# Kernel tuning notes

Measured on AMD Instinct MI355X. Metric: run time of the kernel, lower is better.

Reference implementation:

```python
import jax, jax.numpy as jnp
import numpy as np

BN_EPS = 1e-5
B, CIN, COUT, H, W, K, NSR = 16, 512, 512, 64, 64, 32, 6
M = NSR * K  # 192 codebook centers


def _l2norm(a, axis):
    return a / (1e-6 + jnp.linalg.norm(a, axis=axis, keepdims=True))


def _batchnorm(x, gamma, beta):
    # training-style BN over (batch, H, W), matching SynchronizedBatchNorm2d batch stats
    mean = x.mean(axis=(0, 2, 3), keepdims=True)
    var = x.var(axis=(0, 2, 3), keepdims=True)
    return gamma[None, :, None, None] * (x - mean) * jax.lax.rsqrt(var + BN_EPS) + beta[None, :, None, None]


def setup_inputs() -> dict:
    key = jax.random.key(0)
    ks = jax.random.split(key, 6)
    x = jax.random.normal(ks[0], (B, CIN, H, W), dtype=jnp.float32)
    centers = jax.random.normal(ks[1], (COUT, M), dtype=jnp.float32) * np.sqrt(2.0 / M)
    centers = _l2norm(centers, axis=0)
    # kaiming fan_out init for 1x1 convs
    conv1_w = jax.random.normal(ks[2], (COUT, CIN), dtype=jnp.float32) * np.sqrt(2.0 / COUT)
    conv1_b = jnp.zeros((COUT,), jnp.float32)
    conv2_w = jax.random.normal(ks[3], (CIN, COUT), dtype=jnp.float32) * np.sqrt(2.0 / CIN)
    bn2_g = jnp.ones((CIN,), jnp.float32)
    bn2_b = jnp.zeros((CIN,), jnp.float32)
    conv3_w = jax.random.normal(ks[4], (CIN, CIN), dtype=jnp.float32) * np.sqrt(2.0 / CIN)
    conv3_b = jnp.zeros((CIN,), jnp.float32)
    bn3_g = jnp.ones((CIN,), jnp.float32)
    bn3_b = jnp.zeros((CIN,), jnp.float32)
    return {"x": x, "centers": centers, "conv1_w": conv1_w, "conv1_b": conv1_b,
            "conv2_w": conv2_w, "bn2_g": bn2_g, "bn2_b": bn2_b,
            "conv3_w": conv3_w, "conv3_b": conv3_b, "bn3_g": bn3_g, "bn3_b": bn3_b}


def reference(x, centers, conv1_w, conv1_b, conv2_w, bn2_g, bn2_b, conv3_w, conv3_b, bn3_g, bn3_b):
    b, cin, h, w = x.shape
    # conv1: 1x1 projection in_channels -> out_channels
    x1 = jnp.einsum('oc,bchw->bohw', conv1_w, x) + conv1_b[None, :, None, None]
    x1f = x1.reshape(b, -1, h * w)  # [b, cout, n]
    # attention vs codebook (bases = centers, inference path period=None)
    att = jnp.einsum('bcn,ck->bnk', x1f, centers)  # [b, n, m]
    att = jax.nn.softmax(att, axis=2)
    # double normalization over spatial positions
    att = att / (1e-6 + att.sum(axis=1, keepdims=True))
    # reconstruction from codebook
    x_re = jnp.einsum('bnk,ck->bcn', att, centers).reshape(b, -1, h, w)  # [b, cout, h, w]
    # conv2: 1x1 (no bias) + BN + ReLU, out_channels -> in_channels
    x_re = jax.nn.relu(_batchnorm(jnp.einsum('oc,bchw->bohw', conv2_w, x_re), bn2_g, bn2_b))
    out = x_re + x  # residual
    # conv_bn_dropout: 1x1 conv + BN + ReLU (Dropout2d is identity at eval)
    out = jnp.einsum('oc,bchw->bohw', conv3_w, out) + conv3_b[None, :, None, None]
    out = jax.nn.relu(_batchnorm(out, bn3_g, bn3_b))
    return out
```

## Files before the change

kernel.cpp:

```cpp
#include <hip/hip_runtime.h>
#include <math.h>


#define B_    16
#define C_    512
#define N_    4096
#define M_    192
#define EPS_BN 1e-5f
#define CNT_  ((float)(B_ * N_))

typedef unsigned int   u32;
typedef unsigned short u16;
typedef short bf16x8 __attribute__((ext_vector_type(8)));
typedef float f32x4  __attribute__((ext_vector_type(4)));

__device__ __forceinline__ u16 bf16_rne(float f) {
  u32 u = __float_as_uint(f);
  u += 0x7FFFu + ((u >> 16) & 1u);
  return (u16)(u >> 16);
}
__device__ __forceinline__ float bf16_tof(u16 h) {
  return __uint_as_float(((u32)h) << 16);
}
__device__ __forceinline__ u32 split_pack(float v) {
  u16 h = bf16_rne(v);
  u16 l = bf16_rne(v - bf16_tof(h));
  return (u32)h | ((u32)l << 16);
}
__device__ __forceinline__ void split2(float a, float b, u32& h, u32& l) {
  u16 ha = bf16_rne(a), hb = bf16_rne(b);
  u16 la = bf16_rne(a - bf16_tof(ha)), lb = bf16_rne(b - bf16_tof(hb));
  h = (u32)ha | ((u32)hb << 16);
  l = (u32)la | ((u32)lb << 16);
}

__global__ __launch_bounds__(256) void convert_ew(
    const float* __restrict__ s, u16* __restrict__ hi, u16* __restrict__ lo) {
  const int i = (blockIdx.x * 256 + threadIdx.x) * 4;
  float4 v = *(const float4*)(s + i);
  u32 ph0, pl0, ph1, pl1;
  split2(v.x, v.y, ph0, pl0);
  split2(v.z, v.w, ph1, pl1);
  uint2 H; H.x = ph0; H.y = ph1;
  uint2 L; L.x = pl0; L.y = pl1;
  *(uint2*)(hi + i) = H;
  *(uint2*)(lo + i) = L;
}

__global__ __launch_bounds__(256) void convert_x_T(
    const float* __restrict__ X, u16* __restrict__ Thi, u16* __restrict__ Tlo) {
  __shared__ u32 T[64][65];
  const int tid = threadIdx.x;
  const int n0 = blockIdx.x * 64, c0 = blockIdx.y * 64, b = blockIdx.z;
  const int cg = (tid & 15) * 4;
#pragma unroll
  for (int p = 0; p < 4; ++p) {
    const int r = p * 16 + (tid >> 4);
    float4 v = *(const float4*)(X + ((size_t)b * C_ + c0 + r) * N_ + n0 + cg);
    T[r][cg + 0] = split_pack(v.x);
    T[r][cg + 1] = split_pack(v.y);
    T[r][cg + 2] = split_pack(v.z);
    T[r][cg + 3] = split_pack(v.w);
  }
  __syncthreads();
#pragma unroll
  for (int it = 0; it < 2; ++it) {
    const int s = it * 256 + tid;
    const int nl = s >> 3, cb = s & 7;
    u32 u[8];
#pragma unroll
    for (int j = 0; j < 8; ++j) u[j] = T[cb * 8 + j][nl];
    uint4 H, L;
    H.x = (u[0] & 0xFFFFu) | (u[1] << 16);
    H.y = (u[2] & 0xFFFFu) | (u[3] << 16);
    H.z = (u[4] & 0xFFFFu) | (u[5] << 16);
    H.w = (u[6] & 0xFFFFu) | (u[7] << 16);
    L.x = (u[0] >> 16) | (u[1] & 0xFFFF0000u);
    L.y = (u[2] >> 16) | (u[3] & 0xFFFF0000u);
    L.z = (u[4] >> 16) | (u[5] & 0xFFFF0000u);
    L.w = (u[6] >> 16) | (u[7] & 0xFFFF0000u);
    const size_t o = ((size_t)b * N_ + n0 + nl) * C_ + c0 + cb * 8;
    *(uint4*)(Thi + o) = H;
    *(uint4*)(Tlo + o) = L;
  }
}

__global__ __launch_bounds__(256) void conv_mfma(
    const u16* __restrict__ Whi, const u16* __restrict__ Wlo,
    const u16* __restrict__ Xhi, const u16* __restrict__ Xlo,
    float* __restrict__ Y, const float* __restrict__ bias) {
  __shared__ char sm[32768];
  const int tid = threadIdx.x, wid = tid >> 6, lane = tid & 63;
  const int bn = blockIdx.x * 128, bm = blockIdx.y * 128;
  const size_t boffX = (size_t)blockIdx.z * N_ * C_;
  const size_t boffY = (size_t)blockIdx.z * C_ * N_;

  const u16* srcp[8];
  u32 ldsw[8];
#pragma unroll
  for (int it = 0; it < 8; ++it) {
    const int lin = it * 4 + wid, region = lin >> 3, sub = lin & 7;
    const u16* base = region == 0 ? Whi : region == 1 ? Wlo
                    : region == 2 ? (Xhi + boffX) : (Xlo + boffX);
    const int rowb = (region < 2 ? bm : bn) + sub * 16 + (lane & 15);
    srcp[it] = base + (size_t)rowb * C_ + (lane >> 4) * 8;
    ldsw[it] = (u32)(lin * 1024 + lane * 16);
  }

  f32x4 acc[4][4];
  const f32x4 zero = {0.f, 0.f, 0.f, 0.f};
#pragma unroll
  for (int i = 0; i < 4; ++i)
#pragma unroll
    for (int j = 0; j < 4; ++j) acc[i][j] = zero;

  const int arow = (wid >> 1) * 4, bcol = (wid & 1) * 4;
  const char* smL = sm + lane * 16;

  for (int k0 = 0; k0 < C_; k0 += 32) {
    float4 stg[8];
#pragma unroll
    for (int it = 0; it < 8; ++it) stg[it] = *(const float4*)(srcp[it] + k0);
#pragma unroll
    for (int it = 0; it < 8; ++it) *(float4*)(sm + ldsw[it]) = stg[it];
    __syncthreads();

    bf16x8 ah[4], al[4], bh[4], bl[4];
#pragma unroll
    for (int i = 0; i < 4; ++i) {
      ah[i] = *(const bf16x8*)(smL + (arow + i) * 1024);
      al[i] = *(const bf16x8*)(smL + 8192 + (arow + i) * 1024);
      bh[i] = *(const bf16x8*)(smL + 16384 + (bcol + i) * 1024);
      bl[i] = *(const bf16x8*)(smL + 24576 + (bcol + i) * 1024);
    }
#pragma unroll
    for (int i = 0; i < 4; ++i)
#pragma unroll
      for (int j = 0; j < 4; ++j) {
        acc[i][j] = __builtin_amdgcn_mfma_f32_16x16x32_bf16(ah[i], bh[j], acc[i][j], 0, 0, 0);
        acc[i][j] = __builtin_amdgcn_mfma_f32_16x16x32_bf16(ah[i], bl[j], acc[i][j], 0, 0, 0);
        acc[i][j] = __builtin_amdgcn_mfma_f32_16x16x32_bf16(al[i], bh[j], acc[i][j], 0, 0, 0);
      }
    __syncthreads();
  }

  const int ro = (lane >> 4) * 4, co = lane & 15;
#pragma unroll
  for (int i = 0; i < 4; ++i) {
#pragma unroll
    for (int r = 0; r < 4; ++r) {
      const int o = bm + (wid >> 1) * 64 + i * 16 + ro + r;
      const float bv = bias ? bias[o] : 0.0f;
#pragma unroll
      for (int j = 0; j < 4; ++j) {
        const int n = bn + (wid & 1) * 64 + j * 16 + co;
        Y[boffY + (size_t)o * N_ + n] = acc[i][j][r] + bv;
      }
    }
  }
}

__global__ __launch_bounds__(256) void gemm_att(
    const float* __restrict__ X1, const float* __restrict__ Cent,
    float* __restrict__ Att) {
  const int tid = threadIdx.x;
  const int bn = blockIdx.x * 128;
  const int bk = blockIdx.y * 64;
  const float* Xb = X1 + (size_t)blockIdx.z * C_ * N_;

  __shared__ float As[8][128];
  __shared__ float Bs[8][64];

  float acc[8][4];
#pragma unroll
  for (int i = 0; i < 8; ++i)
#pragma unroll
    for (int j = 0; j < 4; ++j) acc[i][j] = 0.0f;

  const int tm = (tid >> 4) << 3;
  const int tn = (tid & 15) << 2;
  const int a_kc = tid >> 5;
  const int a_m4 = (tid & 31) << 2;
  const int b_kc = tid >> 5;
  const int b_c2 = (tid & 31) << 1;

  for (int k0 = 0; k0 < C_; k0 += 8) {
    *(float4*)&As[a_kc][a_m4] =
        *(const float4*)(Xb + (size_t)(k0 + a_kc) * N_ + bn + a_m4);
    *(float2*)&Bs[b_kc][b_c2] =
        *(const float2*)(Cent + (size_t)(k0 + b_kc) * M_ + bk + b_c2);
    __syncthreads();
#pragma unroll
    for (int kk = 0; kk < 8; ++kk) {
      float ar[8], br[4];
#pragma unroll
      for (int i = 0; i < 8; ++i) ar[i] = As[kk][tm + i];
#pragma unroll
      for (int j = 0; j < 4; ++j) br[j] = Bs[kk][tn + j];
#pragma unroll
      for (int i = 0; i < 8; ++i)
#pragma unroll
        for (int j = 0; j < 4; ++j) acc[i][j] = fmaf(ar[i], br[j], acc[i][j]);
    }
    __syncthreads();
  }

#pragma unroll
  for (int i = 0; i < 8; ++i) {
    float4 o = make_float4(acc[i][0], acc[i][1], acc[i][2], acc[i][3]);
    *(float4*)(Att + ((size_t)blockIdx.z * N_ + bn + tm + i) * M_ + bk + tn) = o;
  }
}

__global__ __launch_bounds__(256) void softmax_rows(float* __restrict__ Att) {
  const int wid  = threadIdx.x >> 6;
  const int lane = threadIdx.x & 63;
  const size_t row = (size_t)blockIdx.x * 4 + wid;
  float* p = Att + row * M_;
  float v0 = p[lane], v1 = p[lane + 64], v2 = p[lane + 128];
  float m = fmaxf(v0, fmaxf(v1, v2));
#pragma unroll
  for (int off = 32; off; off >>= 1) m = fmaxf(m, __shfl_xor(m, off));
  v0 = __expf(v0 - m);
  v1 = __expf(v1 - m);
  v2 = __expf(v2 - m);
  float s = v0 + v1 + v2;
#pragma unroll
  for (int off = 32; off; off >>= 1) s += __shfl_xor(s, off);
  const float r = 1.0f / s;
  p[lane]       = v0 * r;
  p[lane + 64]  = v1 * r;
  p[lane + 128] = v2 * r;
}

__global__ __launch_bounds__(256) void colsum_kernel(
    const float* __restrict__ Att, float* __restrict__ Cs) {
  const int b  = blockIdx.y;
  const int n0 = blockIdx.x * 256;
  const int k  = threadIdx.x;
  if (k < M_) {
    float s = 0.0f;
    const float* p = Att + ((size_t)b * N_ + n0) * M_ + k;
    for (int n = 0; n < 256; ++n) s += p[(size_t)n * M_];
    atomicAdd(&Cs[b * M_ + k], s);
  }
}

__global__ __launch_bounds__(256) void gemm_xre(
    const float* __restrict__ Cent, const float* __restrict__ Att,
    const float* __restrict__ Cs, u16* __restrict__ XThi, u16* __restrict__ XTlo) {
  const int tid = threadIdx.x;
  const int bn = blockIdx.x * 128;
  const int bm = blockIdx.y * 128;
  const int b  = blockIdx.z;

  __shared__ float As[8][128];
  __shared__ float Bs[8][128];
  __shared__ float inv[M_];

  if (tid < M_) inv[tid] = 1.0f / (1e-6f + Cs[b * M_ + tid]);
  __syncthreads();

  float acc[8][8];
#pragma unroll
  for (int i = 0; i < 8; ++i)
#pragma unroll
    for (int j = 0; j < 8; ++j) acc[i][j] = 0.0f;

  const int tm = (tid >> 4) << 3;
  const int tn = (tid & 15) << 3;
  const int a_row = tid >> 1;
  const int a_col = (tid & 1) << 2;
  const int b_row = tid >> 1;
  const int b_col = (tid & 1) << 2;

  for (int k0 = 0; k0 < M_; k0 += 8) {
    float4 av = *(const float4*)(Cent + (size_t)(bm + a_row) * M_ + k0 + a_col);
    As[a_col + 0][a_row] = av.x;
    As[a_col + 1][a_row] = av.y;
    As[a_col + 2][a_row] = av.z;
    As[a_col + 3][a_row] = av.w;
    float4 bv = *(const float4*)(Att + ((size_t)b * N_ + bn + b_row) * M_ + k0 + b_col);
    Bs[b_col + 0][b_row] = bv.x * inv[k0 + b_col + 0];
    Bs[b_col + 1][b_row] = bv.y * inv[k0 + b_col + 1];
    Bs[b_col + 2][b_row] = bv.z * inv[k0 + b_col + 2];
    Bs[b_col + 3][b_row] = bv.w * inv[k0 + b_col + 3];
    __syncthreads();
#pragma unroll
    for (int kk = 0; kk < 8; ++kk) {
      float ar[8], br[8];
#pragma unroll
      for (int i = 0; i < 8; ++i) ar[i] = As[kk][tm + i];
#pragma unroll
      for (int j = 0; j < 8; ++j) br[j] = Bs[kk][tn + j];
#pragma unroll
      for (int i = 0; i < 8; ++i)
#pragma unroll
        for (int j = 0; j < 8; ++j) acc[i][j] = fmaf(ar[i], br[j], acc[i][j]);
    }
    __syncthreads();
  }

#pragma unroll
  for (int jj = 0; jj < 8; ++jj) {
    uint4 H, L;
    split2(acc[0][jj], acc[1][jj], H.x, L.x);
    split2(acc[2][jj], acc[3][jj], H.y, L.y);
    split2(acc[4][jj], acc[5][jj], H.z, L.z);
    split2(acc[6][jj], acc[7][jj], H.w, L.w);
    const size_t o = ((size_t)b * N_ + bn + tn + jj) * C_ + bm + tm;
    *(uint4*)(XThi + o) = H;
    *(uint4*)(XTlo + o) = L;
  }
}

__global__ __launch_bounds__(256) void bnstats(
    const float* __restrict__ Y, float* __restrict__ stats) {
  const int c = blockIdx.x, b = blockIdx.y;
  const float4* p = (const float4*)(Y + ((size_t)b * C_ + c) * N_);
  float s = 0.0f, s2 = 0.0f;
  for (int i = threadIdx.x; i < N_ / 4; i += 256) {
    float4 v = p[i];
    s  += v.x + v.y + v.z + v.w;
    s2 += v.x * v.x + v.y * v.y + v.z * v.z + v.w * v.w;
  }
#pragma unroll
  for (int off = 32; off; off >>= 1) {
    s  += __shfl_xor(s, off);
    s2 += __shfl_xor(s2, off);
  }
  __shared__ float ws[2][4];
  const int lane = threadIdx.x & 63, wid = threadIdx.x >> 6;
  if (lane == 0) { ws[0][wid] = s; ws[1][wid] = s2; }
  __syncthreads();
  if (threadIdx.x == 0) {
    float ts = ws[0][0] + ws[0][1] + ws[0][2] + ws[0][3];
    float t2 = ws[1][0] + ws[1][1] + ws[1][2] + ws[1][3];
    atomicAdd(&stats[c], ts);
    atomicAdd(&stats[C_ + c], t2);
  }
}

__global__ __launch_bounds__(256) void bn_res_T(
    const float* __restrict__ Y, const float* __restrict__ X,
    const float* __restrict__ stats, const float* __restrict__ g,
    const float* __restrict__ bta,
    u16* __restrict__ Thi, u16* __restrict__ Tlo) {
  __shared__ u32 T[64][65];
  const int tid = threadIdx.x;
  const int n0 = blockIdx.x * 64, c0 = blockIdx.y * 64, b = blockIdx.z;
  const int cg = (tid & 15) * 4;
#pragma unroll
  for (int p = 0; p < 4; ++p) {
    const int r = p * 16 + (tid >> 4);
    const int c = c0 + r;
    const float mu  = stats[c] * (1.0f / CNT_);
    const float var = stats[C_ + c] * (1.0f / CNT_) - mu * mu;
    const float rs  = rsqrtf(var + EPS_BN);
    const float ga = g[c], be = bta[c];
    const size_t idx = ((size_t)b * C_ + c) * N_ + n0 + cg;
    float4 v  = *(const float4*)(Y + idx);
    float4 xv = *(const float4*)(X + idx);
    float4 t;
    t.x = fmaxf(ga * (v.x - mu) * rs + be, 0.0f) + xv.x;
    t.y = fmaxf(ga * (v.y - mu) * rs + be, 0.0f) + xv.y;
    t.z = fmaxf(ga * (v.z - mu) * rs + be, 0.0f) + xv.z;
    t.w = fmaxf(ga * (v.w - mu) * rs + be, 0.0f) + xv.w;
    T[r][cg + 0] = split_pack(t.x);
    T[r][cg + 1] = split_pack(t.y);
    T[r][cg + 2] = split_pack(t.z);
    T[r][cg + 3] = split_pack(t.w);
  }
  __syncthreads();
#pragma unroll
  for (int it = 0; it < 2; ++it) {
    const int s = it * 256 + tid;
    const int nl = s >> 3, cb = s & 7;
    u32 u[8];
#pragma unroll
    for (int j = 0; j < 8; ++j) u[j] = T[cb * 8 + j][nl];
    uint4 H, L;
    H.x = (u[0] & 0xFFFFu) | (u[1] << 16);
    H.y = (u[2] & 0xFFFFu) | (u[3] << 16);
    H.z = (u[4] & 0xFFFFu) | (u[5] << 16);
    H.w = (u[6] & 0xFFFFu) | (u[7] << 16);
    L.x = (u[0] >> 16) | (u[1] & 0xFFFF0000u);
    L.y = (u[2] >> 16) | (u[3] & 0xFFFF0000u);
    L.z = (u[4] >> 16) | (u[5] & 0xFFFF0000u);
    L.w = (u[6] >> 16) | (u[7] & 0xFFFF0000u);
    const size_t o = ((size_t)b * N_ + n0 + nl) * C_ + c0 + cb * 8;
    *(uint4*)(Thi + o) = H;
    *(uint4*)(Tlo + o) = L;
  }
}

__global__ __launch_bounds__(256) void bn_apply(
    const float* __restrict__ Y, const float* __restrict__ stats,
    const float* __restrict__ g, const float* __restrict__ bta,
    float* __restrict__ Out) {
  const size_t i = ((size_t)blockIdx.x * 256 + threadIdx.x) * 4;
  const int c = (int)((i >> 12) & (C_ - 1));
  const float mu  = stats[c] * (1.0f / CNT_);
  const float var = stats[C_ + c] * (1.0f / CNT_) - mu * mu;
  const float rs  = rsqrtf(var + EPS_BN);
  const float ga = g[c], be = bta[c];
  float4 y = *(const float4*)(Y + i);
  float4 o;
  o.x = fmaxf(ga * (y.x - mu) * rs + be, 0.0f);
  o.y = fmaxf(ga * (y.y - mu) * rs + be, 0.0f);
  o.z = fmaxf(ga * (y.z - mu) * rs + be, 0.0f);
  o.w = fmaxf(ga * (y.w - mu) * rs + be, 0.0f);
  *(float4*)(Out + i) = o;
}

__global__ __launch_bounds__(256) void zero_small(float* __restrict__ p) {
  p[blockIdx.x * 256 + threadIdx.x] = 0.0f;
}

extern "C" void kernel_launch(void* const* d_in, const int* in_sizes, int n_in,
                              void* d_out, int out_size, void* d_ws, size_t ws_size,
                              hipStream_t stream) {
  const float* x        = (const float*)d_in[0];
  const float* centers  = (const float*)d_in[1];
  const float* conv1_w  = (const float*)d_in[2];
  const float* conv1_b  = (const float*)d_in[3];
  const float* conv2_w  = (const float*)d_in[4];
  const float* bn2_g    = (const float*)d_in[5];
  const float* bn2_b    = (const float*)d_in[6];
  const float* conv3_w  = (const float*)d_in[7];
  const float* conv3_b  = (const float*)d_in[8];
  const float* bn3_g    = (const float*)d_in[9];
  const float* bn3_b    = (const float*)d_in[10];
  float* out = (float*)d_out;

  const size_t TENS = (size_t)B_ * C_ * N_;
  char* w = (char*)d_ws;
  u16* xThi = (u16*)w;
  u16* xTlo = xThi + TENS;
  float* x1 = (float*)(w + 134217728);
  float* att = (float*)(w + 268435456);
  float* colsum = (float*)(w + 268435456 + 50331648);
  float* stats2 = colsum + B_ * M_;
  float* stats3 = stats2 + 2 * C_;
  u16* w1hi = (u16*)(stats3 + 2 * C_);
  u16* w1lo = w1hi + 262144;
  u16* w2hi = w1lo + 262144;
  u16* w2lo = w2hi + 262144;
  u16* w3hi = w2lo + 262144;
  u16* w3lo = w3hi + 262144;
  u16* xreThi = xThi;  u16* xreTlo = xTlo;
  u16* tThi   = xThi;  u16* tTlo   = xTlo;
  float* y2 = x1;

  zero_small<<<20, 256, 0, stream>>>(colsum);
  convert_ew<<<256, 256, 0, stream>>>(conv1_w, w1hi, w1lo);
  convert_ew<<<256, 256, 0, stream>>>(conv2_w, w2hi, w2lo);
  convert_ew<<<256, 256, 0, stream>>>(conv3_w, w3hi, w3lo);
  convert_x_T<<<dim3(N_ / 64, C_ / 64, B_), 256, 0, stream>>>(x, xThi, xTlo);
  conv_mfma<<<dim3(N_ / 128, C_ / 128, B_), 256, 0, stream>>>(
      w1hi, w1lo, xThi, xTlo, x1, conv1_b);
  gemm_att<<<dim3(N_ / 128, M_ / 64, B_), 256, 0, stream>>>(x1, centers, att);
  softmax_rows<<<(B_ * N_) / 4, 256, 0, stream>>>(att);
  colsum_kernel<<<dim3(16, B_), 256, 0, stream>>>(att, colsum);
  gemm_xre<<<dim3(N_ / 128, C_ / 128, B_), 256, 0, stream>>>(
      centers, att, colsum, xreThi, xreTlo);
  conv_mfma<<<dim3(N_ / 128, C_ / 128, B_), 256, 0, stream>>>(
      w2hi, w2lo, xreThi, xreTlo, y2, nullptr);
  bnstats<<<dim3(C_, B_), 256, 0, stream>>>(y2, stats2);
  bn_res_T<<<dim3(N_ / 64, C_ / 64, B_), 256, 0, stream>>>(
      y2, x, stats2, bn2_g, bn2_b, tThi, tTlo);
  conv_mfma<<<dim3(N_ / 128, C_ / 128, B_), 256, 0, stream>>>(
      w3hi, w3lo, tThi, tTlo, out, conv3_b);
  bnstats<<<dim3(C_, B_), 256, 0, stream>>>(out, stats3);
  bn_apply<<<(B_ * C_ * N_) / (4 * 256), 256, 0, stream>>>(
      out, stats3, bn3_g, bn3_b, out);
}
```

Baseline: 1.186 ms.

## Move attention and reconstruction GEMMs to split-bf16 MFMA with fused softmax and colsum

Replaces the fp32 FMA attention GEMM, the separate softmax and colsum kernels, and the fp32 reconstruction GEMM with MFMA kernels using hi/lo bf16 splitting. The conv1 output is now written transposed as split bf16, so the attention kernel computes all 192 logits per position and applies softmax and column-sum atomics in registers. The reconstruction step folds the column normalization into a per-batch scaled copy of the centers and runs through a templated MFMA GEMM. This removes several full passes over the attention tensor and moves slow scalar GEMMs onto matrix cores. The trade-offs are extra atomics, higher register pressure in the attention kernel, and small rounding differences from the 3-term bf16 split.

Measured after the change: 1.120 ms. -5.6%, faster.

```diff
diff --git a/kernel.cpp b/kernel.cpp
--- a/kernel.cpp
+++ b/kernel.cpp
@@ -45,6 +45,32 @@
   uint2 L; L.x = pl0; L.y = pl1;
   *(uint2*)(hi + i) = H;
   *(uint2*)(lo + i) = L;
+}
+
+__global__ __launch_bounds__(256) void centT_conv(
+    const float* __restrict__ cent, u16* __restrict__ hi, u16* __restrict__ lo) {
+  const int idx = blockIdx.x * 256 + threadIdx.x;
+  const int k = idx >> 9, c = idx & 511;
+  const float v = cent[c * M_ + k];
+  u16 h = bf16_rne(v);
+  u16 l = bf16_rne(v - bf16_tof(h));
+  hi[idx] = h;
+  lo[idx] = l;
+}
+
+__global__ __launch_bounds__(256) void cent_scale(
+    const float* __restrict__ cent, const float* __restrict__ colsum,
+    u16* __restrict__ hi, u16* __restrict__ lo) {
+  const int idx = blockIdx.x * 256 + threadIdx.x;
+  const int b = blockIdx.y;
+  const int c = idx / M_;
+  const int k = idx - c * M_;
+  const float v = cent[idx] / (1e-6f + colsum[b * M_ + k]);
+  u16 h = bf16_rne(v);
+  u16 l = bf16_rne(v - bf16_tof(h));
+  const size_t o = (size_t)b * C_ * M_ + idx;
+  hi[o] = h;
+  lo[o] = l;
 }
 
 __global__ __launch_bounds__(256) void convert_x_T(
@@ -85,25 +111,27 @@
   }
 }
 
-__global__ __launch_bounds__(256) void conv_mfma(
-    const u16* __restrict__ Whi, const u16* __restrict__ Wlo,
-    const u16* __restrict__ Xhi, const u16* __restrict__ Xlo,
-    float* __restrict__ Y, const float* __restrict__ bias) {
+template <int KD, int OMODE, bool APB>
+__global__ __launch_bounds__(256) void mm_mfma(
+    const u16* __restrict__ Ahi, const u16* __restrict__ Alo,
+    const u16* __restrict__ Bhi, const u16* __restrict__ Blo,
+    float* __restrict__ Yf, u16* __restrict__ Phi, u16* __restrict__ Plo,
+    const float* __restrict__ bias) {
   __shared__ char sm[32768];
   const int tid = threadIdx.x, wid = tid >> 6, lane = tid & 63;
   const int bn = blockIdx.x * 128, bm = blockIdx.y * 128;
-  const size_t boffX = (size_t)blockIdx.z * N_ * C_;
-  const size_t boffY = (size_t)blockIdx.z * C_ * N_;
+  const size_t boffB = (size_t)blockIdx.z * N_ * KD;
+  const size_t aoff = APB ? (size_t)blockIdx.z * C_ * KD : 0;
 
   const u16* srcp[8];
   u32 ldsw[8];
 #pragma unroll
   for (int it = 0; it < 8; ++it) {
     const int lin = it * 4 + wid, region = lin >> 3, sub = lin & 7;
-    const u16* base = region == 0 ? Whi : region == 1 ? Wlo
-                    : region == 2 ? (Xhi + boffX) : (Xlo + boffX);
+    const u16* base = region == 0 ? (Ahi + aoff) : region == 1 ? (Alo + aoff)
+                    : region == 2 ? (Bhi + boffB) : (Blo + boffB);
     const int rowb = (region < 2 ? bm : bn) + sub * 16 + (lane & 15);
-    srcp[it] = base + (size_t)rowb * C_ + (lane >> 4) * 8;
+    srcp[it] = base + (size_t)rowb * KD + (lane >> 4) * 8;
     ldsw[it] = (u32)(lin * 1024 + lane * 16);
   }
 
@@ -117,7 +145,7 @@
   const int arow = (wid >> 1) * 4, bcol = (wid & 1) * 4;
   const char* smL = sm + lane * 16;
 
-  for (int k0 = 0; k0 < C_; k0 += 32) {
+  for (int k0 = 0; k0 < KD; k0 += 32) {
     float4 stg[8];
 #pragma unroll
     for (int it = 0; it < 8; ++it) stg[it] = *(const float4*)(srcp[it] + k0);
@@ -145,172 +173,155 @@
   }
 
   const int ro = (lane >> 4) * 4, co = lane & 15;
-#pragma unroll
-  for (int i = 0; i < 4; ++i) {
-#pragma unroll
-    for (int r = 0; r < 4; ++r) {
-      const int o = bm + (wid >> 1) * 64 + i * 16 + ro + r;
-      const float bv = bias ? bias[o] : 0.0f;
+  if (OMODE == 0) {
+    const size_t boffY = (size_t)blockIdx.z * C_ * N_;
+#pragma unroll
+    for (int i = 0; i < 4; ++i) {
+#pragma unroll
+      for (int r = 0; r < 4; ++r) {
+        const int o = bm + (wid >> 1) * 64 + i * 16 + ro + r;
+        const float bv = bias ? bias[o] : 0.0f;
+#pragma unroll
+        for (int j = 0; j < 4; ++j) {
+          const int n = bn + (wid & 1) * 64 + j * 16 + co;
+          Yf[boffY + (size_t)o * N_ + n] = acc[i][j][r] + bv;
+        }
+      }
+    }
+  } else {
+#pragma unroll
+    for (int i = 0; i < 4; ++i) {
+      const int ob = bm + (wid >> 1) * 64 + i * 16 + ro;
+      float bv[4];
+#pragma unroll
+      for (int r = 0; r < 4; ++r) bv[r] = bias ? bias[ob + r] : 0.0f;
 #pragma unroll
       for (int j = 0; j < 4; ++j) {
         const int n = bn + (wid & 1) * 64 + j * 16 + co;
-        Y[boffY + (size_t)o * N_ + n] = acc[i][j][r] + bv;
+        u32 h0, l0, h1, l1;
+        split2(acc[i][j][0] + bv[0], acc[i][j][1] + bv[1], h0, l0);
+        split2(acc[i][j][2] + bv[2], acc[i][j][3] + bv[3], h1, l1);
+        const size_t o = ((size_t)blockIdx.z * N_ + n) * C_ + ob;
+        uint2 H; H.x = h0; H.y = h1;
+        uint2 L; L.x = l0; L.y = l1;
+        *(uint2*)(Phi + o) = H;
+        *(uint2*)(Plo + o) = L;
       }
     }
   }
 }
 
-__global__ __launch_bounds__(256) void gemm_att(
-    const float* __restrict__ X1, const float* __restrict__ Cent,
-    float* __restrict__ Att) {
-  const int tid = threadIdx.x;
+__global__ __launch_bounds__(256) void att_mfma(
+    const u16* __restrict__ CThi, const u16* __restrict__ CTlo,
+    const u16* __restrict__ Xhi, const u16* __restrict__ Xlo,
+    u16* __restrict__ Ehi, u16* __restrict__ Elo,
+    float* __restrict__ colsum) {
+  __shared__ char sm[40960];
+  const int tid = threadIdx.x, wid = tid >> 6, lane = tid & 63;
   const int bn = blockIdx.x * 128;
-  const int bk = blockIdx.y * 64;
-  const float* Xb = X1 + (size_t)blockIdx.z * C_ * N_;
-
-  __shared__ float As[8][128];
-  __shared__ float Bs[8][64];
-
-  float acc[8][4];
-#pragma unroll
-  for (int i = 0; i < 8; ++i)
-#pragma unroll
-    for (int j = 0; j < 4; ++j) acc[i][j] = 0.0f;
-
-  const int tm = (tid >> 4) << 3;
-  const int tn = (tid & 15) << 2;
-  const int a_kc = tid >> 5;
-  const int a_m4 = (tid & 31) << 2;
-  const int b_kc = tid >> 5;
-  const int b_c2 = (tid & 31) << 1;
-
-  for (int k0 = 0; k0 < C_; k0 += 8) {
-    *(float4*)&As[a_kc][a_m4] =
-        *(const float4*)(Xb + (size_t)(k0 + a_kc) * N_ + bn + a_m4);
-    *(float2*)&Bs[b_kc][b_c2] =
-        *(const float2*)(Cent + (size_t)(k0 + b_kc) * M_ + bk + b_c2);
+  const int b = blockIdx.z;
+  const size_t bX = (size_t)b * N_ * C_;
+
+  const u16* srcp[10];
+  u32 ldsw[10];
+#pragma unroll
+  for (int it = 0; it < 10; ++it) {
+    const int lin = it * 4 + wid;
+    const u16* base;
+    int rowb;
+    if (lin < 12)      { base = CThi;      rowb = lin * 16 + (lane & 15); }
+    else if (lin < 24) { base = CTlo;      rowb = (lin - 12) * 16 + (lane & 15); }
+    else if (lin < 32) { base = Xhi + bX;  rowb = bn + (lin - 24) * 16 + (lane & 15); }
+    else               { base = Xlo + bX;  rowb = bn + (lin - 32) * 16 + (lane & 15); }
+    srcp[it] = base + (size_t)rowb * C_ + (lane >> 4) * 8;
+    ldsw[it] = (u32)(lin * 1024 + lane * 16);
+  }
+
+  f32x4 acc[12][2];
+  const f32x4 zero = {0.f, 0.f, 0.f, 0.f};
+#pragma unroll
+  for (int i = 0; i < 12; ++i) {
+    acc[i][0] = zero;
+    acc[i][1] = zero;
+  }
+
+  const char* smL = sm + lane * 16;
+
+  for (int k0 = 0; k0 < C_; k0 += 32) {
+    float4 stg[10];
+#pragma unroll
+    for (int it = 0; it < 10; ++it) stg[it] = *(const float4*)(srcp[it] + k0);
+#pragma unroll
+    for (int it = 0; it < 10; ++it) *(float4*)(sm + ldsw[it]) = stg[it];
     __syncthreads();
-#pragma unroll
-    for (int kk = 0; kk < 8; ++kk) {
-      float ar[8], br[4];
-#pragma unroll
-      for (int i = 0; i < 8; ++i) ar[i] = As[kk][tm + i];
-#pragma unroll
-      for (int j = 0; j < 4; ++j) br[j] = Bs[kk][tn + j];
-#pragma unroll
-      for (int i = 0; i < 8; ++i)
-#pragma unroll
-        for (int j = 0; j < 4; ++j) acc[i][j] = fmaf(ar[i], br[j], acc[i][j]);
+
+    bf16x8 bh[2], bl[2];
+#pragma unroll
+    for (int jj = 0; jj < 2; ++jj) {
+      bh[jj] = *(const bf16x8*)(smL + (24 + wid * 2 + jj) * 1024);
+      bl[jj] = *(const bf16x8*)(smL + (32 + wid * 2 + jj) * 1024);
+    }
+#pragma unroll
+    for (int i = 0; i < 12; ++i) {
+      bf16x8 ah = *(const bf16x8*)(smL + i * 1024);
+      bf16x8 al = *(const bf16x8*)(smL + (12 + i) * 1024);
+#pragma unroll
+      for (int jj = 0; jj < 2; ++jj) {
+        acc[i][jj] = __builtin_amdgcn_mfma_f32_16x16x32_bf16(ah, bh[jj], acc[i][jj], 0, 0, 0);
+        acc[i][jj] = __builtin_amdgcn_mfma_f32_16x16x32_bf16(ah, bl[jj], acc[i][jj], 0, 0, 0);
+        acc[i][jj] = __builtin_amdgcn_mfma_f32_16x16x32_bf16(al, bh[jj], acc[i][jj], 0, 0, 0);
+      }
     }
     __syncthreads();
   }
 
-#pragma unroll
-  for (int i = 0; i < 8; ++i) {
-    float4 o = make_float4(acc[i][0], acc[i][1], acc[i][2], acc[i][3]);
-    *(float4*)(Att + ((size_t)blockIdx.z * N_ + bn + tm + i) * M_ + bk + tn) = o;
-  }
-}
-
-__global__ __launch_bounds__(256) void softmax_rows(float* __restrict__ Att) {
-  const int wid  = threadIdx.x >> 6;
-  const int lane = threadIdx.x & 63;
-  const size_t row = (size_t)blockIdx.x * 4 + wid;
-  float* p = Att + row * M_;
-  float v0 = p[lane], v1 = p[lane + 64], v2 = p[lane + 128];
-  float m = fmaxf(v0, fmaxf(v1, v2));
-#pragma unroll
-  for (int off = 32; off; off >>= 1) m = fmaxf(m, __shfl_xor(m, off));
-  v0 = __expf(v0 - m);
-  v1 = __expf(v1 - m);
-  v2 = __expf(v2 - m);
-  float s = v0 + v1 + v2;
-#pragma unroll
-  for (int off = 32; off; off >>= 1) s += __shfl_xor(s, off);
-  const float r = 1.0f / s;
-  p[lane]       = v0 * r;
-  p[lane + 64]  = v1 * r;
-  p[lane + 128] = v2 * r;
-}
-
-__global__ __launch_bounds__(256) void colsum_kernel(
-    const float* __restrict__ Att, float* __restrict__ Cs) {
-  const int b  = blockIdx.y;
-  const int n0 = blockIdx.x * 256;
-  const int k  = threadIdx.x;
-  if (k < M_) {
+  const int ro = (lane >> 4) * 4;
+#pragma unroll
+  for (int jj = 0; jj < 2; ++jj) {
+    const int nn = bn + (wid * 2 + jj) * 16 + (lane & 15);
+    float mx = acc[0][jj][0];
+#pragma unroll
+    for (int i = 0; i < 12; ++i)
+#pragma unroll
+      for (int r = 0; r < 4; ++r) mx = fmaxf(mx, acc[i][jj][r]);
+    mx = fmaxf(mx, __shfl_xor(mx, 16));
+    mx = fmaxf(mx, __shfl_xor(mx, 32));
     float s = 0.0f;
-    const float* p = Att + ((size_t)b * N_ + n0) * M_ + k;
-    for (int n = 0; n < 256; ++n) s += p[(size_t)n * M_];
-    atomicAdd(&Cs[b * M_ + k], s);
-  }
-}
-
-__global__ __launch_bounds__(256) void gemm_xre(
-    const float* __restrict__ Cent, const float* __restrict__ Att,
-    const float* __restrict__ Cs, u16* __restrict__ XThi, u16* __restrict__ XTlo) {
-  const int tid = threadIdx.x;
-  const int bn = blockIdx.x * 128;
-  const int bm = blockIdx.y * 128;
-  const int b  = blockIdx.z;
-
-  __shared__ float As[8][128];
-  __shared__ float Bs[8][128];
-  __shared__ float inv[M_];
-
-  if (tid < M_) inv[tid] = 1.0f / (1e-6f + Cs[b * M_ + tid]);
-  __syncthreads();
-
-  float acc[8][8];
-#pragma unroll
-  for (int i = 0; i < 8; ++i)
-#pragma unroll
-    for (int j = 0; j < 8; ++j) acc[i][j] = 0.0f;
-
-  const int tm = (tid >> 4) << 3;
-  const int tn = (tid & 15) << 3;
-  const int a_row = tid >> 1;
-  const int a_col = (tid & 1) << 2;
-  const int b_row = tid >> 1;
-  const int b_col = (tid & 1) << 2;
-
-  for (int k0 = 0; k0 < M_; k0 += 8) {
-    float4 av = *(const float4*)(Cent + (size_t)(bm + a_row) * M_ + k0 + a_col);
-    As[a_col + 0][a_row] = av.x;
-    As[a_col + 1][a_row] = av.y;
-    As[a_col + 2][a_row] = av.z;
-    As[a_col + 3][a_row] = av.w;
-    float4 bv = *(const float4*)(Att + ((size_t)b * N_ + bn + b_row) * M_ + k0 + b_col);
-    Bs[b_col + 0][b_row] = bv.x * inv[k0 + b_col + 0];
-    Bs[b_col + 1][b_row] = bv.y * inv[k0 + b_col + 1];
-    Bs[b_col + 2][b_row] = bv.z * inv[k0 + b_col + 2];
-    Bs[b_col + 3][b_row] = bv.w * inv[k0 + b_col + 3];
-    __syncthreads();
-#pragma unroll
-    for (int kk = 0; kk < 8; ++kk) {
-      float ar[8], br[8];
-#pragma unroll
-      for (int i = 0; i < 8; ++i) ar[i] = As[kk][tm + i];
-#pragma unroll
-      for (int j = 0; j < 8; ++j) br[j] = Bs[kk][tn + j];
-#pragma unroll
-      for (int i = 0; i < 8; ++i)
-#pragma unroll
-        for (int j = 0; j < 8; ++j) acc[i][j] = fmaf(ar[i], br[j], acc[i][j]);
+#pragma unroll
+    for (int i = 0; i < 12; ++i)
+#pragma unroll
+      for (int r = 0; r < 4; ++r) {
+        const float e = __expf(acc[i][jj][r] - mx);
+        acc[i][jj][r] = e;
+        s += e;
+      }
+    s += __shfl_xor(s, 16);
+    s += __shfl_xor(s, 32);
+    const float rinv = 1.0f / s;
+    const size_t rowo = ((size_t)b * N_ + nn) * M_;
+#pragma unroll
+    for (int i = 0; i < 12; ++i) {
+      float v[4];
+#pragma unroll
+      for (int r = 0; r < 4; ++r) v[r] = acc[i][jj][r] * rinv;
+      u32 h0, l0, h1, l1;
+      split2(v[0], v[1], h0, l0);
+      split2(v[2], v[3], h1, l1);
+      uint2 H; H.x = h0; H.y = h1;
+      uint2 L; L.x = l0; L.y = l1;
+      *(uint2*)(Ehi + rowo + i * 16 + ro) = H;
+      *(uint2*)(Elo + rowo + i * 16 + ro) = L;
+#pragma unroll
+      for (int r = 0; r < 4; ++r) {
+        float t = v[r];
+        t += __shfl_xor(t, 1);
+        t += __shfl_xor(t, 2);
+        t += __shfl_xor(t, 4);
+        t += __shfl_xor(t, 8);
+        if ((lane & 15) == 0)
+          atomicAdd(&colsum[b * M_ + i * 16 + ro + r], t);
+      }
     }
-    __syncthreads();
-  }
-
-#pragma unroll
-  for (int jj = 0; jj < 8; ++jj) {
-    uint4 H, L;
-    split2(acc[0][jj], acc[1][jj], H.x, L.x);
-    split2(acc[2][jj], acc[3][jj], H.y, L.y);
-    split2(acc[4][jj], acc[5][jj], H.z, L.z);
-    split2(acc[6][jj], acc[7][jj], H.w, L.w);
-    const size_t o = ((size_t)b * N_ + bn + tn + jj) * C_ + bm + tm;
-    *(uint4*)(XThi + o) = H;
-    *(uint4*)(XTlo + o) = L;
   }
 }
 
@@ -437,9 +448,17 @@
   char* w = (char*)d_ws;
   u16* xThi = (u16*)w;
   u16* xTlo = xThi + TENS;
-  float* x1 = (float*)(w + 134217728);
-  float* att = (float*)(w + 268435456);
-  float* colsum = (float*)(w + 268435456 + 50331648);
+  char* wB = w + 134217728;
+  u16* x1Thi = (u16*)wB;
+  u16* x1Tlo = x1Thi + TENS;
+  u16* cshi  = (u16*)wB;
+  u16* cslo  = cshi + (size_t)B_ * C_ * M_;
+  float* y2  = (float*)wB;
+  char* wC = w + 268435456;
+  u16* Ehi = (u16*)wC;
+  u16* Elo = Ehi + (size_t)B_ * N_ * M_;
+  char* wD = wC + 50331648;
+  float* colsum = (float*)wD;
   float* stats2 = colsum + B_ * M_;
   float* stats3 = stats2 + 2 * C_;
   u16* w1hi = (u16*)(stats3 + 2 * C_);
@@ -448,29 +467,33 @@
   u16* w2lo = w2hi + 262144;
   u16* w3hi = w2lo + 262144;
   u16* w3lo = w3hi + 262144;
-  u16* xreThi = xThi;  u16* xreTlo = xTlo;
-  u16* tThi   = xThi;  u16* tTlo   = xTlo;
-  float* y2 = x1;
+  u16* cThi = w3lo + 262144;
+  u16* cTlo = cThi + 98304;
+  u16* xreThi = xThi; u16* xreTlo = xTlo;
+  u16* tThi   = xThi; u16* tTlo   = xTlo;
+
+  const dim3 gmm(N_ / 128, C_ / 128, B_);
 
   zero_small<<<20, 256, 0, stream>>>(colsum);
   convert_ew<<<256, 256, 0, stream>>>(conv1_w, w1hi, w1lo);
   convert_ew<<<256, 256, 0, stream>>>(conv2_w, w2hi, w2lo);
   convert_ew<<<256, 256, 0, stream>>>(conv3_w, w3hi, w3lo);
+  centT_conv<<<384, 256, 0, stream>>>(centers, cThi, cTlo);
   convert_x_T<<<dim3(N_ / 64, C_ / 64, B_), 256, 0, stream>>>(x, xThi, xTlo);
-  conv_mfma<<<dim3(N_ / 128, C_ / 128, B_), 256, 0, stream>>>(
-      w1hi, w1lo, xThi, xTlo, x1, conv1_b);
-  gemm_att<<<dim3(N_ / 128, M_ / 64, B_), 256, 0, stream>>>(x1, centers, att);
-  softmax_rows<<<(B_ * N_) / 4, 256, 0, stream>>>(att);
-  colsum_kernel<<<dim3(16, B_), 256, 0, stream>>>(att, colsum);
-  gemm_xre<<<dim3(N_ / 128, C_ / 128, B_), 256, 0, stream>>>(
-      centers, att, colsum, xreThi, xreTlo);
-  conv_mfma<<<dim3(N_ / 128, C_ / 128, B_), 256, 0, stream>>>(
-      w2hi, w2lo, xreThi, xreTlo, y2, nullptr);
+  mm_mfma<512, 1, false><<<gmm, 256, 0, stream>>>(
+      w1hi, w1lo, xThi, xTlo, nullptr, x1Thi, x1Tlo, conv1_b);
+  att_mfma<<<dim3(N_ / 128, 1, B_), 256, 0, stream>>>(
+      cThi, cTlo, x1Thi, x1Tlo, Ehi, Elo, colsum);
+  cent_scale<<<dim3(384, B_), 256, 0, stream>>>(centers, colsum, cshi, cslo);
+  mm_mfma<192, 1, true><<<gmm, 256, 0, stream>>>(
+      cshi, cslo, Ehi, Elo, nullptr, xreThi, xreTlo, nullptr);
+  mm_mfma<512, 0, false><<<gmm, 256, 0, stream>>>(
+      w2hi, w2lo, xreThi, xreTlo, y2, nullptr, nullptr, nullptr);
   bnstats<<<dim3(C_, B_), 256, 0, stream>>>(y2, stats2);
   bn_res_T<<<dim3(N_ / 64, C_ / 64, B_), 256, 0, stream>>>(
       y2, x, stats2, bn2_g, bn2_b, tThi, tTlo);
-  conv_mfma<<<dim3(N_ / 128, C_ / 128, B_), 256, 0, stream>>>(
-      w3hi, w3lo, tThi, tTlo, out, conv3_b);
+  mm_mfma<512, 0, false><<<gmm, 256, 0, stream>>>(
+      w3hi, w3lo, tThi, tTlo, out, nullptr, nullptr, conv3_b);
   bnstats<<<dim3(C_, B_), 256, 0, stream>>>(out, stats3);
   bn_apply<<<(B_ * C_ * N_) / (4 * 256), 256, 0, stream>>>(
       out, stats3, bn3_g, bn3_b, out);
```
